# Performance work log

Hardware: AMD Instinct MI355X
Metric: run time of the kernel (lower is better)

## Reference

```python
import jax, jax.numpy as jnp
import numpy as np

ALPHA = 0.2
NEG_INF = -9e15


def setup_inputs() -> dict:
    key = jax.random.key(0)
    k1, k2, k3, k4 = jax.random.split(key, 4)
    N, F_IN, F_OUT, H = 4096, 1, 64, 12
    x = jax.random.normal(k1, (N, F_IN), dtype=jnp.float32)
    adj = jax.random.randint(k2, (N, N), 0, 2).astype(jnp.int32)
    # per-head params stacked: W [H, F_IN, F_OUT], a [H, 2*F_OUT, 1]
    W = jax.random.normal(k3, (H, F_IN, F_OUT), dtype=jnp.float32) * 0.1
    a = jax.random.normal(k4, (H, 2 * F_OUT, 1), dtype=jnp.float32) * 0.1
    return {"x": x, "adj": adj, "W": W, "a": a}


def reference(x, adj, W, a):
    # h per head: [H, N, F_OUT]
    h = jnp.einsum('nf,hfo->hno', x, W)
    F_out = h.shape[-1]
    # a_input[i,j] = concat(h_i, h_j), so a_input @ a = h_i.a_src + h_j.a_dst
    a_src = a[:, :F_out, 0]   # [H, F_OUT]
    a_dst = a[:, F_out:, 0]   # [H, F_OUT]
    e_src = jnp.einsum('hnf,hf->hn', h, a_src)  # [H, N]
    e_dst = jnp.einsum('hnf,hf->hn', h, a_dst)  # [H, N]
    e = jax.nn.leaky_relu(e_src[:, :, None] + e_dst[:, None, :], ALPHA)  # [H,N,N]
    e = jnp.where(adj[None] > 0, e, NEG_INF)
    attn = jax.nn.softmax(e, axis=-1)           # softmax over neighbors j
    h_prime = jnp.einsum('hij,hjf->hif', attn, h)  # [H, N, F_OUT]
    # concat heads along feature dim -> [N, H*F_OUT]
    N = h_prime.shape[1]
    return jnp.transpose(h_prime, (1, 0, 2)).reshape(N, -1)
```

## Files before the change

### kernel.cpp

```cpp
#include <hip/hip_runtime.h>

#define GAT_H 12
#define GAT_N 4096
#define GAT_F 64
#define LOG2E 1.4426950408889634f


__device__ float2 g_tab[GAT_H * GAT_N];
__device__ float  g_sd[2 * GAT_H + 1];

__global__ __launch_bounds__(256) void gat_prep(const float* __restrict__ W,
                                                const float* __restrict__ a,
                                                const float* __restrict__ x) {
    const int b    = blockIdx.x;
    const int tid  = threadIdx.x;
    const int lane = tid & 63;
    const int wave = tid >> 6;

    if (b < GAT_H) {
        if (wave == 0) {
            const float wf = W[b * GAT_F + lane];
            float ps = wf * a[b * 2 * GAT_F + lane];
            float pd = wf * a[b * 2 * GAT_F + GAT_F + lane];
            #pragma unroll
            for (int off = 32; off > 0; off >>= 1) {
                ps += __shfl_xor(ps, off, 64);
                pd += __shfl_xor(pd, off, 64);
            }
            if (lane == 0) { g_sd[b] = ps; g_sd[GAT_H + b] = pd; }
        }
        return;
    }
    if (b == GAT_H) {
        if (wave == 0) {
            float s = 0.0f;
            #pragma unroll
            for (int j = 0; j < GAT_N / 64; ++j) s += x[j * 64 + lane];
            #pragma unroll
            for (int off = 32; off > 0; off >>= 1) s += __shfl_xor(s, off, 64);
            if (lane == 0) g_sd[2 * GAT_H] = s * (1.0f / GAT_N);
        }
        return;
    }

    const int bt    = b - (GAT_H + 1);
    const int h     = bt >> 2;
    const int chunk = bt & 3;
    const float wf  = W[h * GAT_F + lane];
    float pd = wf * a[h * 2 * GAT_F + GAT_F + lane];
    #pragma unroll
    for (int off = 32; off > 0; off >>= 1) pd += __shfl_xor(pd, off, 64);
    const float dl = pd * LOG2E;
    #pragma unroll
    for (int k = 0; k < 4; ++k) {
        const int j   = chunk * 1024 + k * 256 + tid;
        const float t = dl * x[j];
        g_tab[h * GAT_N + j] = make_float2(__builtin_amdgcn_exp2f(t),
                                           __builtin_amdgcn_exp2f(0.2f * t));
    }
}

__global__ __launch_bounds__(256, 4) void gat_main(const float* __restrict__ x,
                                                   const int* __restrict__ adj,
                                                   const float* __restrict__ W,
                                                   float* __restrict__ out) {
    __shared__ float xs[GAT_N];
    __shared__ float rho_s[4][16];
    __shared__ float part[2][2][4][6][2];
    __shared__ float cbuf[4][GAT_H];

    const int tid  = threadIdx.x;
    const int row0 = blockIdx.x * 4;

    #pragma unroll
    for (int it = 0; it < GAT_N / (256 * 4); ++it)
        ((float4*)xs)[it * 256 + tid] = ((const float4*)x)[it * 256 + tid];
    if (tid < 64) {
        const int r = tid >> 4, hh = tid & 15;
        if (hh < GAT_H)
            rho_s[r][hh] =
                __builtin_amdgcn_exp2f(-0.8f * LOG2E * x[row0 + r] * g_sd[hh]);
    }
    __syncthreads();

    const int lane  = tid & 63;
    const int wave  = tid >> 6;
    const int hg    = wave >> 1;
    const int jh    = wave & 1;
    const int hbase = hg * 6;
    const int jb    = jh * 2048 + lane;

    float rho[4][6];
    #pragma unroll
    for (int r = 0; r < 4; ++r)
        #pragma unroll
        for (int hh = 0; hh < 6; ++hh)
            rho[r][hh] = __uint_as_float(__builtin_amdgcn_readfirstlane(
                __float_as_uint(rho_s[r][hbase + hh])));

    float den[4][6], num[4][6];
    #pragma unroll
    for (int r = 0; r < 4; ++r)
        #pragma unroll
        for (int hh = 0; hh < 6; ++hh) { den[r][hh] = 0.0f; num[r][hh] = 0.0f; }

    const int*    __restrict__ adp = adj + (size_t)row0 * GAT_N + jb;
    const float2* __restrict__ tb  = g_tab + hbase * GAT_N + jb;

    int    a_c[4];
    float2 E_c[6];
    float  x_c;
    #pragma unroll
    for (int r = 0; r < 4; ++r)  a_c[r]  = adp[r * GAT_N];
    #pragma unroll
    for (int hh = 0; hh < 6; ++hh) E_c[hh] = tb[hh * GAT_N];
    x_c = xs[jb];

    #pragma unroll 2
    for (int e = 0; e < 32; ++e) {
        const int eo = (e < 31 ? e + 1 : 31) * 64;
        int    a_n[4];
        float2 E_n[6];
        #pragma unroll
        for (int r = 0; r < 4; ++r)   a_n[r]  = adp[r * GAT_N + eo];
        #pragma unroll
        for (int hh = 0; hh < 6; ++hh) E_n[hh] = tb[hh * GAT_N + eo];
        const float x_n = xs[jb + eo];

        float m[4], mxj[4];
        #pragma unroll
        for (int r = 0; r < 4; ++r) {
            const bool nb = a_c[r] > 0;
            m[r]   = nb ? 1.0f : 0.0f;
            mxj[r] = nb ? x_c  : 0.0f;
        }
        #pragma unroll
        for (int hh = 0; hh < 6; ++hh) {
            const float e1 = E_c[hh].x, e2 = E_c[hh].y;
            #pragma unroll
            for (int r = 0; r < 4; ++r) {
                const float p = fmaxf(e1, rho[r][hh] * e2);
                den[r][hh] = fmaf(p, m[r],   den[r][hh]);
                num[r][hh] = fmaf(p, mxj[r], num[r][hh]);
            }
        }
        #pragma unroll
        for (int r = 0; r < 4; ++r)   a_c[r]  = a_n[r];
        #pragma unroll
        for (int hh = 0; hh < 6; ++hh) E_c[hh] = E_n[hh];
        x_c = x_n;
    }

    #pragma unroll
    for (int r = 0; r < 4; ++r) {
        #pragma unroll
        for (int hh = 0; hh < 6; ++hh) {
            float d = den[r][hh], n = num[r][hh];
            #pragma unroll
            for (int off = 32; off > 0; off >>= 1) {
                d += __shfl_xor(d, off, 64);
                n += __shfl_xor(n, off, 64);
            }
            if (lane == 0) {
                part[jh][hg][r][hh][0] = d;
                part[jh][hg][r][hh][1] = n;
            }
        }
    }
    __syncthreads();

    if (tid < 64) {
        const int r = tid >> 4, h = tid & 15;
        if (h < GAT_H) {
            const int g  = (h >= 6) ? 1 : 0;
            const int hh = h - 6 * g;
            const float dsum = part[0][g][r][hh][0] + part[1][g][r][hh][0];
            const float nsum = part[0][g][r][hh][1] + part[1][g][r][hh][1];
            cbuf[r][h] = dsum > 0.0f ? nsum / dsum : g_sd[2 * GAT_H];
        }
    }
    __syncthreads();

    #pragma unroll
    for (int r = 0; r < 4; ++r) {
        const size_t base = (size_t)(row0 + r) * (GAT_H * GAT_F);
        #pragma unroll
        for (int k = 0; k < 3; ++k) {
            const int pos = k * 256 + tid;
            out[base + pos] = cbuf[r][pos >> 6] * W[pos];
        }
    }
}

extern "C" void kernel_launch(void* const* d_in, const int* in_sizes, int n_in,
                              void* d_out, int out_size, void* d_ws, size_t ws_size,
                              hipStream_t stream) {
    const float* x   = (const float*)d_in[0];
    const int*   adj = (const int*)d_in[1];
    const float* W   = (const float*)d_in[2];
    const float* a   = (const float*)d_in[3];
    float* out = (float*)d_out;
    (void)d_ws; (void)ws_size;

    gat_prep<<<GAT_H + 1 + 48, 256, 0, stream>>>(W, a, x);
    gat_main<<<GAT_N / 4, 256, 0, stream>>>(x, adj, W, out);
}
```

Baseline: 143.9 us.

## Pack adjacency into bitmasks in prep kernel, read bits in main loop

Adds 512 blocks to the prep kernel that ballot each 64-column slice of the int32 adjacency matrix into a 64-bit mask stored in a global bitmap. The main kernel then reads these uniform mask words instead of per-lane int adjacency values, and extracts its neighbour flag with a shift. The adjacency matrix is still read once in full, so total traffic is unchanged and an extra 2 MB bitmap write and reread is added. The main kernel's launch bounds also drop from 4 to 3 waves per SIMD and its loop unroll from 2 to 1.

```diff
diff --git a/kernel.cpp b/kernel.cpp
--- a/kernel.cpp
+++ b/kernel.cpp
@@ -3,15 +3,18 @@
 #define GAT_H 12
 #define GAT_N 4096
 #define GAT_F 64
+#define GAT_NW (GAT_N / 64)
 #define LOG2E 1.4426950408889634f
 
 
 __device__ float2 g_tab[GAT_H * GAT_N];
 __device__ float  g_sd[2 * GAT_H + 1];
+__device__ unsigned long long g_bits[GAT_N * GAT_NW];
 
 __global__ __launch_bounds__(256) void gat_prep(const float* __restrict__ W,
                                                 const float* __restrict__ a,
-                                                const float* __restrict__ x) {
+                                                const float* __restrict__ x,
+                                                const int* __restrict__ adj) {
     const int b    = blockIdx.x;
     const int tid  = threadIdx.x;
     const int lane = tid & 63;
@@ -42,26 +45,40 @@
         }
         return;
     }
-
-    const int bt    = b - (GAT_H + 1);
-    const int h     = bt >> 2;
-    const int chunk = bt & 3;
-    const float wf  = W[h * GAT_F + lane];
-    float pd = wf * a[h * 2 * GAT_F + GAT_F + lane];
-    #pragma unroll
-    for (int off = 32; off > 0; off >>= 1) pd += __shfl_xor(pd, off, 64);
-    const float dl = pd * LOG2E;
-    #pragma unroll
-    for (int k = 0; k < 4; ++k) {
-        const int j   = chunk * 1024 + k * 256 + tid;
-        const float t = dl * x[j];
-        g_tab[h * GAT_N + j] = make_float2(__builtin_amdgcn_exp2f(t),
-                                           __builtin_amdgcn_exp2f(0.2f * t));
+    if (b < GAT_H + 1 + 48) {
+        const int bt    = b - (GAT_H + 1);
+        const int h     = bt >> 2;
+        const int chunk = bt & 3;
+        const float wf  = W[h * GAT_F + lane];
+        float pd = wf * a[h * 2 * GAT_F + GAT_F + lane];
+        #pragma unroll
+        for (int off = 32; off > 0; off >>= 1) pd += __shfl_xor(pd, off, 64);
+        const float dl = pd * LOG2E;
+        #pragma unroll
+        for (int k = 0; k < 4; ++k) {
+            const int j   = chunk * 1024 + k * 256 + tid;
+            const float t = dl * x[j];
+            g_tab[h * GAT_N + j] = make_float2(__builtin_amdgcn_exp2f(t),
+                                               __builtin_amdgcn_exp2f(0.2f * t));
+        }
+        return;
+    }
+
+    const int bp  = b - (GAT_H + 1 + 48);
+    const int row = bp * 8 + wave * 2;
+    #pragma unroll
+    for (int rr = 0; rr < 2; ++rr) {
+        const int r = row + rr;
+        const int* __restrict__ ar = adj + (size_t)r * GAT_N;
+        #pragma unroll 4
+        for (int it = 0; it < GAT_NW; ++it) {
+            const unsigned long long mask = __ballot(ar[it * 64 + lane] > 0);
+            if (lane == 0) g_bits[r * GAT_NW + it] = mask;
+        }
     }
 }
 
-__global__ __launch_bounds__(256, 4) void gat_main(const float* __restrict__ x,
-                                                   const int* __restrict__ adj,
+__global__ __launch_bounds__(256, 3) void gat_main(const float* __restrict__ x,
                                                    const float* __restrict__ W,
                                                    float* __restrict__ out) {
     __shared__ float xs[GAT_N];
@@ -104,33 +121,33 @@
         #pragma unroll
         for (int hh = 0; hh < 6; ++hh) { den[r][hh] = 0.0f; num[r][hh] = 0.0f; }
 
-    const int*    __restrict__ adp = adj + (size_t)row0 * GAT_N + jb;
-    const float2* __restrict__ tb  = g_tab + hbase * GAT_N + jb;
-
-    int    a_c[4];
+    const float2* __restrict__ tb = g_tab + hbase * GAT_N + jb;
+    const unsigned long long* __restrict__ bp0 =
+        g_bits + (size_t)row0 * GAT_NW + jh * 32;
+
     float2 E_c[6];
-    float  x_c;
-    #pragma unroll
-    for (int r = 0; r < 4; ++r)  a_c[r]  = adp[r * GAT_N];
+    unsigned long long b_c[4];
     #pragma unroll
     for (int hh = 0; hh < 6; ++hh) E_c[hh] = tb[hh * GAT_N];
-    x_c = xs[jb];
-
-    #pragma unroll 2
+    #pragma unroll
+    for (int r = 0; r < 4; ++r)    b_c[r]  = bp0[r * GAT_NW];
+    float x_c = xs[jb];
+
+    #pragma unroll 1
     for (int e = 0; e < 32; ++e) {
-        const int eo = (e < 31 ? e + 1 : 31) * 64;
-        int    a_n[4];
+        const int en = (e < 31) ? e + 1 : 31;
         float2 E_n[6];
-        #pragma unroll
-        for (int r = 0; r < 4; ++r)   a_n[r]  = adp[r * GAT_N + eo];
-        #pragma unroll
-        for (int hh = 0; hh < 6; ++hh) E_n[hh] = tb[hh * GAT_N + eo];
-        const float x_n = xs[jb + eo];
+        unsigned long long b_n[4];
+        #pragma unroll
+        for (int hh = 0; hh < 6; ++hh) E_n[hh] = tb[hh * GAT_N + en * 64];
+        #pragma unroll
+        for (int r = 0; r < 4; ++r)    b_n[r]  = bp0[r * GAT_NW + en];
+        const float x_n = xs[jb + en * 64];
 
         float m[4], mxj[4];
         #pragma unroll
         for (int r = 0; r < 4; ++r) {
-            const bool nb = a_c[r] > 0;
+            const bool nb = (b_c[r] >> lane) & 1ull;
             m[r]   = nb ? 1.0f : 0.0f;
             mxj[r] = nb ? x_c  : 0.0f;
         }
@@ -145,9 +162,9 @@
             }
         }
         #pragma unroll
-        for (int r = 0; r < 4; ++r)   a_c[r]  = a_n[r];
-        #pragma unroll
         for (int hh = 0; hh < 6; ++hh) E_c[hh] = E_n[hh];
+        #pragma unroll
+        for (int r = 0; r < 4; ++r)    b_c[r]  = b_n[r];
         x_c = x_n;
     }
 
@@ -202,6 +219,6 @@
     float* out = (float*)d_out;
     (void)d_ws; (void)ws_size;
 
-    gat_prep<<<GAT_H + 1 + 48, 256, 0, stream>>>(W, a, x);
-    gat_main<<<GAT_N / 4, 256, 0, stream>>>(x, adj, W, out);
+    gat_prep<<<GAT_H + 1 + 48 + 512, 256, 0, stream>>>(W, a, x, adj);
+    gat_main<<<GAT_N / 4, 256, 0, stream>>>(x, W, out);
 }
```

New measurement: 204.4 us. 42.0% more time.

## Store only exp2 of scaled dst term and vectorize adjacency/table loads

Applied to the files above, without the earlier changes.

The prep table now holds a single float per (head,node), exp2(0.2*d*x), and the main kernel recovers the other factor as its fifth power with two multiplies, halving table traffic. The main loop reads adjacency, table and x as float4/int4 vectors, four columns per lane per iteration, in 8 iterations instead of 32. The adjacency mask is built by converting the int directly to float, which assumes adj holds only 0/1. Occupancy hint drops from 4 to 3 blocks per CU to give more registers. Computing the fifth power can overflow or lose precision for large exponents, and loads of the table are no longer prefetched one iteration ahead.

```diff
diff --git a/kernel.cpp b/kernel.cpp
--- a/kernel.cpp
+++ b/kernel.cpp
@@ -6,8 +6,8 @@
 #define LOG2E 1.4426950408889634f
 
 
-__device__ float2 g_tab[GAT_H * GAT_N];
-__device__ float  g_sd[2 * GAT_H + 1];
+__device__ float g_tab2[GAT_H * GAT_N];
+__device__ float g_sd[2 * GAT_H + 1];
 
 __global__ __launch_bounds__(256) void gat_prep(const float* __restrict__ W,
                                                 const float* __restrict__ a,
@@ -50,17 +50,15 @@
     float pd = wf * a[h * 2 * GAT_F + GAT_F + lane];
     #pragma unroll
     for (int off = 32; off > 0; off >>= 1) pd += __shfl_xor(pd, off, 64);
-    const float dl = pd * LOG2E;
+    const float dl5 = 0.2f * pd * LOG2E;
     #pragma unroll
     for (int k = 0; k < 4; ++k) {
-        const int j   = chunk * 1024 + k * 256 + tid;
-        const float t = dl * x[j];
-        g_tab[h * GAT_N + j] = make_float2(__builtin_amdgcn_exp2f(t),
-                                           __builtin_amdgcn_exp2f(0.2f * t));
+        const int j = chunk * 1024 + k * 256 + tid;
+        g_tab2[h * GAT_N + j] = __builtin_amdgcn_exp2f(dl5 * x[j]);
     }
 }
 
-__global__ __launch_bounds__(256, 4) void gat_main(const float* __restrict__ x,
+__global__ __launch_bounds__(256, 3) void gat_main(const float* __restrict__ x,
                                                    const int* __restrict__ adj,
                                                    const float* __restrict__ W,
                                                    float* __restrict__ out) {
@@ -88,7 +86,6 @@
     const int hg    = wave >> 1;
     const int jh    = wave & 1;
     const int hbase = hg * 6;
-    const int jb    = jh * 2048 + lane;
 
     float rho[4][6];
     #pragma unroll
@@ -104,51 +101,59 @@
         #pragma unroll
         for (int hh = 0; hh < 6; ++hh) { den[r][hh] = 0.0f; num[r][hh] = 0.0f; }
 
-    const int*    __restrict__ adp = adj + (size_t)row0 * GAT_N + jb;
-    const float2* __restrict__ tb  = g_tab + hbase * GAT_N + jb;
-
-    int    a_c[4];
-    float2 E_c[6];
-    float  x_c;
-    #pragma unroll
-    for (int r = 0; r < 4; ++r)  a_c[r]  = adp[r * GAT_N];
-    #pragma unroll
-    for (int hh = 0; hh < 6; ++hh) E_c[hh] = tb[hh * GAT_N];
-    x_c = xs[jb];
-
-    #pragma unroll 2
-    for (int e = 0; e < 32; ++e) {
-        const int eo = (e < 31 ? e + 1 : 31) * 64;
-        int    a_n[4];
-        float2 E_n[6];
-        #pragma unroll
-        for (int r = 0; r < 4; ++r)   a_n[r]  = adp[r * GAT_N + eo];
-        #pragma unroll
-        for (int hh = 0; hh < 6; ++hh) E_n[hh] = tb[hh * GAT_N + eo];
-        const float x_n = xs[jb + eo];
-
-        float m[4], mxj[4];
+    const int4*   __restrict__ a4p = (const int4*)(adj + (size_t)row0 * GAT_N + jh * 2048);
+    const float4* __restrict__ t4  = (const float4*)(g_tab2 + hbase * GAT_N + jh * 2048);
+    const float4* __restrict__ x4  = (const float4*)(xs + jh * 2048);
+
+    int4   ac[4];
+    float4 xc;
+    #pragma unroll
+    for (int r = 0; r < 4; ++r) ac[r] = a4p[r * (GAT_N / 4) + lane];
+    xc = x4[lane];
+
+    #pragma unroll 1
+    for (int it = 0; it < 8; ++it) {
+        const int nxt = (it < 7 ? it + 1 : 7) * 64 + lane;
+        int4 an[4];
+        #pragma unroll
+        for (int r = 0; r < 4; ++r) an[r] = a4p[r * (GAT_N / 4) + nxt];
+        const float4 xn = x4[nxt];
+
+        float am[4][4], axj[4][4];
         #pragma unroll
         for (int r = 0; r < 4; ++r) {
-            const bool nb = a_c[r] > 0;
-            m[r]   = nb ? 1.0f : 0.0f;
-            mxj[r] = nb ? x_c  : 0.0f;
-        }
+            const int* ai = (const int*)&ac[r];
+            const float* xv = (const float*)&xc;
+            #pragma unroll
+            for (int e = 0; e < 4; ++e) {
+                am[r][e]  = (float)ai[e];
+                axj[r][e] = am[r][e] * xv[e];
+            }
+        }
+
         #pragma unroll
         for (int hh = 0; hh < 6; ++hh) {
-            const float e1 = E_c[hh].x, e2 = E_c[hh].y;
-            #pragma unroll
-            for (int r = 0; r < 4; ++r) {
-                const float p = fmaxf(e1, rho[r][hh] * e2);
-                den[r][hh] = fmaf(p, m[r],   den[r][hh]);
-                num[r][hh] = fmaf(p, mxj[r], num[r][hh]);
-            }
-        }
-        #pragma unroll
-        for (int r = 0; r < 4; ++r)   a_c[r]  = a_n[r];
-        #pragma unroll
-        for (int hh = 0; hh < 6; ++hh) E_c[hh] = E_n[hh];
-        x_c = x_n;
+            const float4 e2v = t4[hh * (GAT_N / 4) + it * 64 + lane];
+            const float* e2 = (const float*)&e2v;
+            float e1[4];
+            #pragma unroll
+            for (int e = 0; e < 4; ++e) {
+                const float sq = e2[e] * e2[e];
+                e1[e] = sq * sq * e2[e];
+            }
+            #pragma unroll
+            for (int e = 0; e < 4; ++e) {
+                #pragma unroll
+                for (int r = 0; r < 4; ++r) {
+                    const float p = fmaxf(e1[e], rho[r][hh] * e2[e]);
+                    den[r][hh] = fmaf(p, am[r][e],  den[r][hh]);
+                    num[r][hh] = fmaf(p, axj[r][e], num[r][hh]);
+                }
+            }
+        }
+        #pragma unroll
+        for (int r = 0; r < 4; ++r) ac[r] = an[r];
+        xc = xn;
     }
 
     #pragma unroll
```

Result: faster. 133.2 us (-7.4%).
